# Performance work log

Measured on AMD Instinct MI355X. Metric: run time of the kernel, lower is better.

## Reference

```python
import jax, jax.numpy as jnp
import numpy as np

P = 65536          # collocation points
J = 16             # num_subdomains == pou num_partitions
WID = 64           # subnet width_size
N_SUB_HID = 2      # subnet depth=3 -> 2 extra hidden linear layers after the input layer
H = 64             # pou hidden_dim
N_POU_RES = 4      # pou depth=6 -> 4 residual blocks


def setup_inputs() -> dict:
    key = jax.random.key(0)
    ks = jax.random.split(key, 14)
    s = 0.1  # small init scale for stable tanh/softmax
    return {
        "x": jax.random.uniform(ks[0], (P, 2), jnp.float32),
        "sub_W0": s * jax.random.normal(ks[1], (J, 2, WID), jnp.float32),
        "sub_b0": s * jax.random.normal(ks[2], (J, WID), jnp.float32),
        "sub_Wh": s * jax.random.normal(ks[3], (J, N_SUB_HID, WID, WID), jnp.float32),
        "sub_bh": s * jax.random.normal(ks[4], (J, N_SUB_HID, WID), jnp.float32),
        "sub_Wl": s * jax.random.normal(ks[5], (J, WID, 1), jnp.float32),
        "sub_bl": s * jax.random.normal(ks[6], (J, 1), jnp.float32),
        "pou_W0": s * jax.random.normal(ks[7], (2, H), jnp.float32),
        "pou_b0": s * jax.random.normal(ks[8], (H,), jnp.float32),
        "pou_Wh": s * jax.random.normal(ks[9], (N_POU_RES, H, H), jnp.float32),
        "pou_bh": s * jax.random.normal(ks[10], (N_POU_RES, H), jnp.float32),
        "pou_Wl": s * jax.random.normal(ks[11], (H, J), jnp.float32),
        "pou_bl": s * jax.random.normal(ks[12], (J,), jnp.float32),
    }


def reference(x, sub_W0, sub_b0, sub_Wh, sub_bh, sub_Wl, sub_bl,
              pou_W0, pou_b0, pou_Wh, pou_bh, pou_Wl, pou_bl):
    x = jnp.atleast_2d(x)
    # --- ResPOUNet2D.forward: partition-of-unity weights (computed ONCE, not per j) ---
    h = jax.nn.relu(x @ pou_W0 + pou_b0)                      # [P, H]
    for i in range(pou_Wh.shape[0]):                          # residual relu blocks
        h = h + jax.nn.relu(h @ pou_Wh[i] + pou_bh[i])
    w_all = jax.nn.softmax(h @ pou_Wl + pou_bl, axis=-1)      # [P, J]
    # --- batched subnets: eqx.nn.MLP with tanh, applied to (x-0.5)*2 ---
    xs = (x - 0.5) * 2.0                                      # [P, 2]
    hs = jnp.tanh(jnp.einsum('pd,jdw->jpw', xs, sub_W0) + sub_b0[:, None, :])  # [J, P, W]
    for i in range(sub_Wh.shape[1]):
        hs = jnp.tanh(jnp.einsum('jpw,jwv->jpv', hs, sub_Wh[:, i]) + sub_bh[:, i][:, None, :])
    u = (jnp.einsum('jpw,jwo->jpo', hs, sub_Wl) + sub_bl[:, None, :])[..., 0]  # [J, P]
    # --- weighted sum over subdomains ---
    total = jnp.einsum('pj,jp->p', w_all, u)                  # [P]
    # --- ansatz: hard zero-Dirichlet BC on unit square ---
    return total * jnp.sin(jnp.pi * x[:, 0]) * jnp.sin(jnp.pi * x[:, 1])
```

## Files before the change

kernel.cpp:

```cpp
#include <hip/hip_runtime.h>
#include <math.h>

#define NP 65536
#define NJ 16
#define WID 64
#define HH 64
#define NPOU 4
#define NSUB 2
#define L2E2 2.8853900817779268f

typedef __attribute__((ext_vector_type(8))) short short8;
typedef __attribute__((ext_vector_type(4))) float f32x4;
typedef __attribute__((ext_vector_type(4))) int int4v;

#define CHUNK_US(row, chunk) ((((row) << 6)) + ((((chunk) ^ ((row) & 7))) << 3))
__device__ __forceinline__ int usIdx(int row, int col) {
    return ((row) << 6) + ((((col >> 3) ^ (row & 7))) << 3) + (col & 7);
}

__device__ __forceinline__ unsigned short f2bf(float f) {
    unsigned u = __float_as_uint(f);
    u += 0x7FFFu + ((u >> 16) & 1u);
    return (unsigned short)(u >> 16);
}
__device__ __forceinline__ unsigned short rhu(float f) {
    return (unsigned short)((__float_as_uint(f) + 0x8000u) >> 16);
}
__device__ __forceinline__ unsigned pk2(float a, float b) {
    unsigned ua = __float_as_uint(a) + 0x8000u;
    unsigned ub = __float_as_uint(b) + 0x8000u;
    return __builtin_amdgcn_perm(ub, ua, 0x07060302u);
}
__device__ __forceinline__ unsigned cvtpk(float a, float b) {
    unsigned r;
    asm("v_cvt_pk_bf16_f32 %0, %1, %2" : "=v"(r) : "v"(a), "v"(b));
    return r;
}
__device__ __forceinline__ float bf2f(unsigned short s) {
    return __uint_as_float(((unsigned)s) << 16);
}
__device__ __forceinline__ float tanh2(float y) {
    float e = __builtin_amdgcn_exp2f(y);
    return fmaf(-2.0f, __builtin_amdgcn_rcpf(e + 1.0f), 1.0f);
}
__device__ __forceinline__ short8 mk8(unsigned a, unsigned b, unsigned c, unsigned d) {
    int4v t; t.x = (int)a; t.y = (int)b; t.z = (int)c; t.w = (int)d;
    return __builtin_bit_cast(short8, t);
}
#define CB_TRANSFORM(hsrc, bfdst)                                              \
    {                                                                          \
        _Pragma("unroll")                                                      \
        for (int kn = 0; kn < 2; ++kn) {                                       \
            unsigned A0 = cvtpk(hsrc[2 * kn][0],     hsrc[2 * kn][1]);         \
            unsigned A1 = cvtpk(hsrc[2 * kn][2],     hsrc[2 * kn][3]);         \
            unsigned B0 = cvtpk(hsrc[2 * kn + 1][0], hsrc[2 * kn + 1][1]);     \
            unsigned B1 = cvtpk(hsrc[2 * kn + 1][2], hsrc[2 * kn + 1][3]);     \
            asm("v_permlane32_swap_b32 %0, %1" : "+v"(A0), "+v"(B0));          \
            asm("v_permlane16_swap_b32 %0, %1" : "+v"(A0), "+v"(B0));          \
            asm("v_permlane32_swap_b32 %0, %1" : "+v"(A1), "+v"(B1));          \
            asm("v_permlane16_swap_b32 %0, %1" : "+v"(A1), "+v"(B1));          \
            bfdst[kn] = mk8(A0, A1, B0, B1);                                   \
        }                                                                      \
    }

__global__ __launch_bounds__(256) void prep_all_kernel(
    const float* __restrict__ sW0, const float* __restrict__ sb0,
    const float* __restrict__ sWh, const float* __restrict__ sbh_,
    const float* __restrict__ sWl, const float* __restrict__ sbl,
    const float* __restrict__ pW0, const float* __restrict__ pb0,
    const float* __restrict__ pWh, const float* __restrict__ pbh,
    const float* __restrict__ pWl, const float* __restrict__ pbl,
    int4v* __restrict__ wfrag, float* __restrict__ prm,
    int4v* __restrict__ pwf,   float* __restrict__ pp)
{
    const int blk = blockIdx.x;
    const int tid = threadIdx.x;

    if (blk < 64) {
        const int j  = blk >> 2;
        const int bx = blk & 3;
        const int f  = bx * 256 + tid;
        const int lane = f & 63, kc = (f >> 6) & 1, mt = (f >> 7) & 3, L = f >> 9;
        const int c = lane & 15, g = lane >> 4;
        const int n = mt * 16 + c;

        const float* src = sWh + j * (NSUB * WID * WID) + L * 4096;
        unsigned w[4];
#pragma unroll
        for (int e2 = 0; e2 < 4; ++e2) {
            int k = kc * 32 + 8 * g + 2 * e2;
            float v0 = L2E2 * src[k * 64 + n];
            float v1 = L2E2 * src[(k + 1) * 64 + n];
            w[e2] = (unsigned)f2bf(v0) | ((unsigned)f2bf(v1) << 16);
        }
        int4v r; r.x = (int)w[0]; r.y = (int)w[1]; r.z = (int)w[2]; r.w = (int)w[3];
        wfrag[j * 1024 + f] = r;

        if (bx == 0) {
            float* pj = prm + j * 512;
            if (tid < WID) {
                float w0 = sW0[j * 2 * WID + tid], w1 = sW0[j * 2 * WID + WID + tid];
                pj[tid]       = 2.0f * L2E2 * w0;
                pj[64 + tid]  = 2.0f * L2E2 * w1;
                pj[128 + tid] = L2E2 * (sb0[j * WID + tid] - w0 - w1);
            }
            if (tid < NSUB * WID) pj[192 + tid] = L2E2 * sbh_[j * NSUB * WID + tid];
            if (tid < WID) pj[320 + tid] = sWl[j * WID + tid];
            if (tid == 0) pj[384] = sbl[j];
        }
    } else {
        const int pb = blk - 64;
        const int idx = pb * 256 + tid;

        if (idx < 2048) {
            const int r = idx >> 9, mt = (idx >> 7) & 3, kc = (idx >> 6) & 1, lane = idx & 63;
            const int c = lane & 15, g = lane >> 4;
            const int n = mt * 16 + c;
            const float* src = pWh + r * 4096;
            unsigned w[4];
#pragma unroll
            for (int e2 = 0; e2 < 4; ++e2) {
                int k = kc * 32 + 8 * g + 2 * e2;
                w[e2] = (unsigned)f2bf(src[k * 64 + n]) | ((unsigned)f2bf(src[(k + 1) * 64 + n]) << 16);
            }
            int4v rr; rr.x = (int)w[0]; rr.y = (int)w[1]; rr.z = (int)w[2]; rr.w = (int)w[3];
            pwf[idx] = rr;
        } else if (idx < 2176) {
            const int t = idx - 2048;
            const int kc = t >> 6, lane = t & 63;
            const int jj = lane & 15, g = lane >> 4;
            unsigned w[4];
#pragma unroll
            for (int e2 = 0; e2 < 4; ++e2) {
                int k = kc * 32 + 8 * g + 2 * e2;
                w[e2] = (unsigned)f2bf(pWl[k * 16 + jj]) | ((unsigned)f2bf(pWl[(k + 1) * 16 + jj]) << 16);
            }
            int4v rr; rr.x = (int)w[0]; rr.y = (int)w[1]; rr.z = (int)w[2]; rr.w = (int)w[3];
            pwf[idx] = rr;
        }
        if (pb == 8) {
            if (tid < HH) {
                pp[tid]       = pW0[tid];
                pp[64 + tid]  = pW0[HH + tid];
                pp[128 + tid] = pb0[tid];
            }
            pp[192 + tid] = pbh[tid];
            if (tid < NJ) pp[448 + tid] = pbl[tid];
        }
    }
}

__global__ __launch_bounds__(256) void pou16_kernel(
    const float* __restrict__ x,
    const short8* __restrict__ pwf, const float* __restrict__ pp,
    float* __restrict__ w_all)
{
    const int tid = threadIdx.x, wave = tid >> 6, lane = tid & 63;
    const int c = lane & 15, g = lane >> 4;
    const int pb = blockIdx.x * 64 + wave * 16;

    float2 xv = ((const float2*)x)[pb + c];

    float trunk[4][4];
#pragma unroll
    for (int mt = 0; mt < 4; ++mt) {
        f32x4 a  = *(const f32x4*)&pp[      mt * 16 + 4 * g];
        f32x4 b  = *(const f32x4*)&pp[ 64 + mt * 16 + 4 * g];
        f32x4 bb = *(const f32x4*)&pp[128 + mt * 16 + 4 * g];
#pragma unroll
        for (int q = 0; q < 4; ++q)
            trunk[mt][q] = fmaxf(fmaf(xv.x, a[q], fmaf(xv.y, b[q], bb[q])), 0.0f);
    }

#pragma unroll
    for (int r = 0; r < NPOU; ++r) {
        short8 bf[2];
        CB_TRANSFORM(trunk, bf);
        f32x4 acc[4];
#pragma unroll
        for (int mt = 0; mt < 4; ++mt)
            acc[mt] = *(const f32x4*)&pp[192 + r * 64 + mt * 16 + 4 * g];
#pragma unroll
        for (int mt = 0; mt < 4; ++mt) {
            short8 a0 = pwf[((r * 4 + mt) * 2 + 0) * 64 + lane];
            short8 a1 = pwf[((r * 4 + mt) * 2 + 1) * 64 + lane];
            acc[mt] = __builtin_amdgcn_mfma_f32_16x16x32_bf16(a0, bf[0], acc[mt], 0, 0, 0);
            acc[mt] = __builtin_amdgcn_mfma_f32_16x16x32_bf16(a1, bf[1], acc[mt], 0, 0, 0);
        }
#pragma unroll
        for (int mt = 0; mt < 4; ++mt)
#pragma unroll
            for (int q = 0; q < 4; ++q)
                trunk[mt][q] += fmaxf(acc[mt][q], 0.0f);
    }

    short8 bfl[2];
    CB_TRANSFORM(trunk, bfl);
    f32x4 lac = *(const f32x4*)&pp[448 + 4 * g];
    lac = __builtin_amdgcn_mfma_f32_16x16x32_bf16(pwf[2048 + lane],      bfl[0], lac, 0, 0, 0);
    lac = __builtin_amdgcn_mfma_f32_16x16x32_bf16(pwf[2048 + 64 + lane], bfl[1], lac, 0, 0, 0);

    float m = fmaxf(fmaxf(lac[0], lac[1]), fmaxf(lac[2], lac[3]));
    m = fmaxf(m, __shfl_xor(m, 16));
    m = fmaxf(m, __shfl_xor(m, 32));
    float ev[4]; float s = 0.0f;
#pragma unroll
    for (int q = 0; q < 4; ++q) { ev[q] = __expf(lac[q] - m); s += ev[q]; }
    s += __shfl_xor(s, 16);
    s += __shfl_xor(s, 32);
    const float ss = __builtin_amdgcn_sinf(xv.x * 0.5f) * __builtin_amdgcn_sinf(xv.y * 0.5f);
    const float f = __builtin_amdgcn_rcpf(s) * ss;
#pragma unroll
    for (int q = 0; q < 4; ++q)
        w_all[(4 * g + q) * NP + pb + c] = ev[q] * f;
}

__global__ __launch_bounds__(256, 4) void subnet_nolds_kernel(
    const float* __restrict__ x,
    const short8* __restrict__ wfrag,
    const float* __restrict__ prm,
    const float* __restrict__ w_all,
    float* __restrict__ out)
{
    const int tid  = threadIdx.x;
    const int j    = blockIdx.y;
    const int wave = tid >> 6;
    const int lane = tid & 63;
    const int c    = lane & 15;
    const int g    = lane >> 4;

    const float*  pj = prm + j * 512;
    const short8* wf = wfrag + j * 1024;
    const int pb = blockIdx.x * 256 + wave * 64;

    short8 bf[2][4];
    {
        float xs0[4], xs1[4];
#pragma unroll
        for (int nt = 0; nt < 4; ++nt) {
            float2 xv = ((const float2*)x)[pb + nt * 16 + c];
            xs0[nt] = xv.x; xs1[nt] = xv.y;
        }
        f32x4 wa[2][2], wb[2][2], bb[2][2];
#pragma unroll
        for (int kc = 0; kc < 2; ++kc)
#pragma unroll
            for (int hf = 0; hf < 2; ++hf) {
                wa[kc][hf] = *(const f32x4*)&pj[      kc * 32 + 8 * g + 4 * hf];
                wb[kc][hf] = *(const f32x4*)&pj[ 64 + kc * 32 + 8 * g + 4 * hf];
                bb[kc][hf] = *(const f32x4*)&pj[128 + kc * 32 + 8 * g + 4 * hf];
            }
        unsigned t[2][4][4];
#pragma unroll
        for (int kc = 0; kc < 2; ++kc)
#pragma unroll
            for (int pr = 0; pr < 4; ++pr) {
                const int h0 = pr >> 1, e0 = (2 * pr) & 3, e1 = e0 + 1;
#pragma unroll
                for (int nt = 0; nt < 4; ++nt) {
                    float v0 = tanh2(fmaf(xs0[nt], wa[kc][h0][e0], fmaf(xs1[nt], wb[kc][h0][e0], bb[kc][h0][e0])));
                    float v1 = tanh2(fmaf(xs0[nt], wa[kc][h0][e1], fmaf(xs1[nt], wb[kc][h0][e1], bb[kc][h0][e1])));
                    t[kc][nt][pr] = cvtpk(v0, v1);
                }
            }
#pragma unroll
        for (int kc = 0; kc < 2; ++kc)
#pragma unroll
            for (int nt = 0; nt < 4; ++nt)
                bf[kc][nt] = mk8(t[kc][nt][0], t[kc][nt][1], t[kc][nt][2], t[kc][nt][3]);
    }

    float red[4];
#pragma unroll
    for (int nt = 0; nt < 4; ++nt) red[nt] = 0.0f;

#pragma unroll
    for (int L = 0; L < NSUB; ++L) {
        short8 aw[4][2];
#pragma unroll
        for (int mt = 0; mt < 4; ++mt)
#pragma unroll
            for (int kc = 0; kc < 2; ++kc)
                aw[mt][kc] = wf[((L * 4 + mt) * 2 + kc) * 64 + lane];
        f32x4 bias[4];
#pragma unroll
        for (int mt = 0; mt < 4; ++mt)
            bias[mt] = *(const f32x4*)&pj[192 + L * 64 + mt * 16 + 4 * g];

#pragma unroll
        for (int nt = 0; nt < 4; ++nt) {
            f32x4 acc[4];
#pragma unroll
            for (int mt = 0; mt < 4; ++mt) acc[mt] = bias[mt];
#pragma unroll
            for (int mt = 0; mt < 4; ++mt) {
                acc[mt] = __builtin_amdgcn_mfma_f32_16x16x32_bf16(aw[mt][0], bf[0][nt], acc[mt], 0, 0, 0);
                acc[mt] = __builtin_amdgcn_mfma_f32_16x16x32_bf16(aw[mt][1], bf[1][nt], acc[mt], 0, 0, 0);
            }

            if (L < NSUB - 1) {
                float h[4][4];
#pragma unroll
                for (int mt = 0; mt < 4; ++mt)
#pragma unroll
                    for (int q = 0; q < 4; ++q) h[mt][q] = tanh2(acc[mt][q]);
                short8 btmp[2];
                CB_TRANSFORM(h, btmp);
                bf[0][nt] = btmp[0];
                bf[1][nt] = btmp[1];
            } else {
#pragma unroll
                for (int mt = 0; mt < 4; ++mt) {
                    f32x4 wlv = *(const f32x4*)&pj[320 + mt * 16 + 4 * g];
#pragma unroll
                    for (int q = 0; q < 4; ++q)
                        red[nt] = fmaf(tanh2(acc[mt][q]), wlv[q], red[nt]);
                }
            }
        }
    }

#pragma unroll
    for (int nt = 0; nt < 4; ++nt) {
        red[nt] += __shfl_xor(red[nt], 16);
        red[nt] += __shfl_xor(red[nt], 32);
    }
    float u = (g & 1) ? ((g & 2) ? red[3] : red[1]) : ((g & 2) ? red[2] : red[0]);
    u += pj[384];

    const int p = pb + lane;
    atomicAdd(&out[p], u * w_all[j * NP + p]);
}

__global__ __launch_bounds__(256) void pou_mfma_kernel(
    const float* __restrict__ x,
    const float* __restrict__ W0, const float* __restrict__ b0,
    const float* __restrict__ Wh, const float* __restrict__ bh,
    const float* __restrict__ Wl, const float* __restrict__ bl,
    float* __restrict__ w_all)
{
    __shared__ unsigned short sA[4 * 64 * 64];
    __shared__ unsigned short sWhT[NPOU * 64 * 64];
    __shared__ unsigned short sWlT[16 * 64];
    __shared__ float sW0a[HH], sW0b[HH], sB0[HH];
    __shared__ float sbh[NPOU * HH];
    __shared__ float sbl[NJ];

    const int tid  = threadIdx.x;
    const int wave = tid >> 6;
    const int lane = tid & 63;
    const int r15  = lane & 15;
    const int g    = lane >> 4;

    for (int idx = tid; idx < NPOU * HH * HH; idx += 256) {
        int r = idx >> 12, k = (idx >> 6) & 63, n = idx & 63;
        sWhT[r * 4096 + usIdx(n, k)] = f2bf(Wh[idx]);
    }
    for (int idx = tid; idx < HH * NJ; idx += 256) {
        int k = idx >> 4, j = idx & 15;
        sWlT[usIdx(j, k)] = f2bf(Wl[idx]);
    }
    if (tid < HH) { sW0a[tid] = W0[tid]; sW0b[tid] = W0[HH + tid]; sB0[tid] = b0[tid]; }
    for (int i = tid; i < NPOU * HH; i += 256) sbh[i] = bh[i];
    if (tid < NJ) sbl[tid] = bl[tid];
    __syncthreads();

    unsigned short* myA = &sA[wave * 4096];
    const int pbase = blockIdx.x * 256;

    {
        const int p = pbase + tid;
        float2 xv = ((const float2*)x)[p];
        float v[HH];
#pragma unroll
        for (int c = 0; c < HH; ++c)
            v[c] = fmaxf(fmaf(xv.x, sW0a[c], fmaf(xv.y, sW0b[c], sB0[c])), 0.0f);
#pragma unroll
        for (int c = 0; c < 8; ++c) {
            int4v r;
            r.x = (int)pk2(v[8 * c + 0], v[8 * c + 1]);
            r.y = (int)pk2(v[8 * c + 2], v[8 * c + 3]);
            r.z = (int)pk2(v[8 * c + 4], v[8 * c + 5]);
            r.w = (int)pk2(v[8 * c + 6], v[8 * c + 7]);
            *(int4v*)&myA[CHUNK_US(lane, c)] = r;
        }
    }

    float trunk[4][4][4];
#pragma unroll
    for (int mt = 0; mt < 4; ++mt)
#pragma unroll
        for (int nt = 0; nt < 4; ++nt)
#pragma unroll
            for (int q = 0; q < 4; ++q)
                trunk[mt][nt][q] = bf2f(myA[usIdx(mt * 16 + g * 4 + q, nt * 16 + r15)]);

#pragma unroll 1
    for (int r = 0; r < NPOU; ++r) {
        const unsigned short* wt = &sWhT[r * 4096];
        short8 bfr[2][4];
#pragma unroll
        for (int kc = 0; kc < 2; ++kc)
#pragma unroll
            for (int nt = 0; nt < 4; ++nt)
                bfr[kc][nt] = *(const short8*)&wt[CHUNK_US(nt * 16 + r15, kc * 4 + g)];
        float bias[4];
#pragma unroll
        for (int nt = 0; nt < 4; ++nt) bias[nt] = sbh[r * HH + nt * 16 + r15];

#pragma unroll
        for (int mt = 0; mt < 4; ++mt) {
            short8 a0 = *(const short8*)&myA[CHUNK_US(mt * 16 + r15, g)];
            short8 a1 = *(const short8*)&myA[CHUNK_US(mt * 16 + r15, 4 + g)];
            f32x4 acc[4];
#pragma unroll
            for (int nt = 0; nt < 4; ++nt) {
                acc[nt] = (f32x4)(0.0f);
                acc[nt] = __builtin_amdgcn_mfma_f32_16x16x32_bf16(a0, bfr[0][nt], acc[nt], 0, 0, 0);
                acc[nt] = __builtin_amdgcn_mfma_f32_16x16x32_bf16(a1, bfr[1][nt], acc[nt], 0, 0, 0);
            }
#pragma unroll
            for (int nt = 0; nt < 4; ++nt)
#pragma unroll
                for (int q = 0; q < 4; ++q) {
                    float t = trunk[mt][nt][q] + fmaxf(acc[nt][q] + bias[nt], 0.0f);
                    trunk[mt][nt][q] = t;
                    myA[usIdx(mt * 16 + g * 4 + q, nt * 16 + r15)] = rhu(t);
                }
        }
    }

    short8 bw0 = *(const short8*)&sWlT[CHUNK_US(r15, g)];
    short8 bw1 = *(const short8*)&sWlT[CHUNK_US(r15, 4 + g)];
    float lg[4][4], mx[4][4];
#pragma unroll
    for (int mt = 0; mt < 4; ++mt) {
        short8 a0 = *(const short8*)&myA[CHUNK_US(mt * 16 + r15, g)];
        short8 a1 = *(const short8*)&myA[CHUNK_US(mt * 16 + r15, 4 + g)];
        f32x4 acc = (f32x4)(0.0f);
        acc = __builtin_amdgcn_mfma_f32_16x16x32_bf16(a0, bw0, acc, 0, 0, 0);
        acc = __builtin_amdgcn_mfma_f32_16x16x32_bf16(a1, bw1, acc, 0, 0, 0);
#pragma unroll
        for (int q = 0; q < 4; ++q) { lg[mt][q] = acc[q] + sbl[r15]; mx[mt][q] = lg[mt][q]; }
    }
#pragma unroll
    for (int mask = 1; mask < 16; mask <<= 1)
#pragma unroll
        for (int mt = 0; mt < 4; ++mt)
#pragma unroll
            for (int q = 0; q < 4; ++q) mx[mt][q] = fmaxf(mx[mt][q], __shfl_xor(mx[mt][q], mask));
    float ev[4][4], sm[4][4];
#pragma unroll
    for (int mt = 0; mt < 4; ++mt)
#pragma unroll
        for (int q = 0; q < 4; ++q) { ev[mt][q] = __expf(lg[mt][q] - mx[mt][q]); sm[mt][q] = ev[mt][q]; }
#pragma unroll
    for (int mask = 1; mask < 16; mask <<= 1)
#pragma unroll
        for (int mt = 0; mt < 4; ++mt)
#pragma unroll
            for (int q = 0; q < 4; ++q) sm[mt][q] += __shfl_xor(sm[mt][q], mask);
#pragma unroll
    for (int mt = 0; mt < 4; ++mt)
#pragma unroll
        for (int q = 0; q < 4; ++q) {
            const int p = pbase + wave * 64 + mt * 16 + g * 4 + q;
            w_all[r15 * NP + p] = ev[mt][q] * __builtin_amdgcn_rcpf(sm[mt][q]);
        }
}

__global__ __launch_bounds__(256) void subnet_mfma_fallback(
    const float* __restrict__ x,
    const float* __restrict__ gW0, const float* __restrict__ gb0,
    const float* __restrict__ gWh, const float* __restrict__ gbh,
    const float* __restrict__ gWl, const float* __restrict__ gbl,
    const float* __restrict__ w_all,
    float* __restrict__ upart)
{
    __shared__ __align__(16) unsigned short sWt[NSUB * 64 * 64];
    __shared__ __align__(16) float sW0a[WID], sW0b[WID], sB0[WID];
    __shared__ __align__(16) float sbh[NSUB * WID];
    __shared__ __align__(16) float sWl[WID];
    __shared__ float sbl1v;

    const int tid  = threadIdx.x;
    const int j    = blockIdx.y;
    const int wave = tid >> 6;
    const int lane = tid & 63;
    const int c    = lane & 15;
    const int g    = lane >> 4;

    {
        const float* src = gWh + j * (NSUB * WID * WID);
        for (int idx = tid; idx < NSUB * WID * WID; idx += 256) {
            int L = idx >> 12, rem = idx & 4095;
            int k = rem >> 6, n = rem & 63;
            sWt[L * 4096 + usIdx(n, k)] = f2bf(L2E2 * src[idx]);
        }
        if (tid < WID) {
            float w0 = gW0[j * 2 * WID + tid], w1 = gW0[j * 2 * WID + WID + tid];
            sW0a[tid] = 2.0f * L2E2 * w0;
            sW0b[tid] = 2.0f * L2E2 * w1;
            sB0[tid]  = L2E2 * (gb0[j * WID + tid] - w0 - w1);
        }
        if (tid < NSUB * WID) sbh[tid] = L2E2 * gbh[j * NSUB * WID + tid];
        if (tid < WID) sWl[tid] = gWl[j * WID + tid];
        if (tid == 0) sbl1v = gbl[j];
    }
    __syncthreads();

    const int pb = blockIdx.x * 256 + wave * 64;

    short8 bf[2][4];
    {
        float xs0[4], xs1[4];
#pragma unroll
        for (int nt = 0; nt < 4; ++nt) {
            float2 xv = ((const float2*)x)[pb + nt * 16 + c];
            xs0[nt] = xv.x; xs1[nt] = xv.y;
        }
        f32x4 wa[2][2], wb[2][2], bb[2][2];
#pragma unroll
        for (int kc = 0; kc < 2; ++kc)
#pragma unroll
            for (int hf = 0; hf < 2; ++hf) {
                wa[kc][hf] = *(const f32x4*)&sW0a[kc * 32 + 8 * g + 4 * hf];
                wb[kc][hf] = *(const f32x4*)&sW0b[kc * 32 + 8 * g + 4 * hf];
                bb[kc][hf] = *(const f32x4*)&sB0 [kc * 32 + 8 * g + 4 * hf];
            }
        unsigned t[2][4][4];
#pragma unroll
        for (int kc = 0; kc < 2; ++kc)
#pragma unroll
            for (int pr = 0; pr < 4; ++pr) {
                const int h0 = pr >> 1, e0 = (2 * pr) & 3, e1 = e0 + 1;
#pragma unroll
                for (int nt = 0; nt < 4; ++nt) {
                    float v0 = tanh2(fmaf(xs0[nt], wa[kc][h0][e0], fmaf(xs1[nt], wb[kc][h0][e0], bb[kc][h0][e0])));
                    float v1 = tanh2(fmaf(xs0[nt], wa[kc][h0][e1], fmaf(xs1[nt], wb[kc][h0][e1], bb[kc][h0][e1])));
                    t[kc][nt][pr] = cvtpk(v0, v1);
                }
            }
#pragma unroll
        for (int kc = 0; kc < 2; ++kc)
#pragma unroll
            for (int nt = 0; nt < 4; ++nt)
                bf[kc][nt] = mk8(t[kc][nt][0], t[kc][nt][1], t[kc][nt][2], t[kc][nt][3]);
    }

    float red[4];
#pragma unroll
    for (int nt = 0; nt < 4; ++nt) red[nt] = 0.0f;

#pragma unroll
    for (int L = 0; L < NSUB; ++L) {
        const unsigned short* wt = &sWt[L * 4096];
        short8 aw[4][2];
#pragma unroll
        for (int mt = 0; mt < 4; ++mt)
#pragma unroll
            for (int kc = 0; kc < 2; ++kc)
                aw[mt][kc] = *(const short8*)&wt[CHUNK_US(mt * 16 + c, kc * 4 + g)];
        f32x4 bias[4];
#pragma unroll
        for (int mt = 0; mt < 4; ++mt)
            bias[mt] = *(const f32x4*)&sbh[L * 64 + mt * 16 + 4 * g];

#pragma unroll
        for (int nt = 0; nt < 4; ++nt) {
            f32x4 acc[4];
#pragma unroll
            for (int mt = 0; mt < 4; ++mt) acc[mt] = bias[mt];
#pragma unroll
            for (int mt = 0; mt < 4; ++mt) {
                acc[mt] = __builtin_amdgcn_mfma_f32_16x16x32_bf16(aw[mt][0], bf[0][nt], acc[mt], 0, 0, 0);
                acc[mt] = __builtin_amdgcn_mfma_f32_16x16x32_bf16(aw[mt][1], bf[1][nt], acc[mt], 0, 0, 0);
            }

            if (L < NSUB - 1) {
                float h[4][4];
#pragma unroll
                for (int mt = 0; mt < 4; ++mt)
#pragma unroll
                    for (int q = 0; q < 4; ++q) h[mt][q] = tanh2(acc[mt][q]);
                short8 btmp[2];
                CB_TRANSFORM(h, btmp);
                bf[0][nt] = btmp[0];
                bf[1][nt] = btmp[1];
            } else {
#pragma unroll
                for (int mt = 0; mt < 4; ++mt) {
                    f32x4 wlv = *(const f32x4*)&sWl[mt * 16 + 4 * g];
#pragma unroll
                    for (int q = 0; q < 4; ++q)
                        red[nt] = fmaf(tanh2(acc[mt][q]), wlv[q], red[nt]);
                }
            }
        }
    }

#pragma unroll
    for (int nt = 0; nt < 4; ++nt) {
        red[nt] += __shfl_xor(red[nt], 16);
        red[nt] += __shfl_xor(red[nt], 32);
    }
    float u = (g & 1) ? ((g & 2) ? red[3] : red[1]) : ((g & 2) ? red[2] : red[0]);
    u += sbl1v;

    const int p = pb + lane;
    upart[j * NP + p] = u * w_all[j * NP + p];
}

__global__ __launch_bounds__(256) void reduce_kernel(
    const float* __restrict__ x,
    const float* __restrict__ upart,
    float* __restrict__ out)
{
    const int p = blockIdx.x * 256 + threadIdx.x;
    float s = 0.0f;
#pragma unroll
    for (int j = 0; j < NJ; ++j) s += upart[j * NP + p];
    float2 xv = ((const float2*)x)[p];
    float s0 = __builtin_amdgcn_sinf(xv.x * 0.5f);
    float s1 = __builtin_amdgcn_sinf(xv.y * 0.5f);
    out[p] = s * s0 * s1;
}

extern "C" void kernel_launch(void* const* d_in, const int* in_sizes, int n_in,
                              void* d_out, int out_size, void* d_ws, size_t ws_size,
                              hipStream_t stream) {
    const float* x      = (const float*)d_in[0];
    const float* sub_W0 = (const float*)d_in[1];
    const float* sub_b0 = (const float*)d_in[2];
    const float* sub_Wh = (const float*)d_in[3];
    const float* sub_bh = (const float*)d_in[4];
    const float* sub_Wl = (const float*)d_in[5];
    const float* sub_bl = (const float*)d_in[6];
    const float* pou_W0 = (const float*)d_in[7];
    const float* pou_b0 = (const float*)d_in[8];
    const float* pou_Wh = (const float*)d_in[9];
    const float* pou_bh = (const float*)d_in[10];
    const float* pou_Wl = (const float*)d_in[11];
    const float* pou_bl = (const float*)d_in[12];

    float* w_all = (float*)d_ws;
    float* upart = (float*)d_ws + (size_t)NJ * NP;
    char*  extra  = (char*)d_ws + (size_t)2 * NJ * NP * 4;
    void*  swf    = (void*)extra;
    float* sprm   = (float*)(extra + (size_t)NJ * 1024 * 16);
    char*  extra2 = extra + (size_t)NJ * 1024 * 16 + (size_t)NJ * 512 * 4;
    void*  pwf    = (void*)extra2;
    float* pprm   = (float*)(extra2 + 2176 * 16);

    const size_t need = (size_t)2 * NJ * NP * 4 + (size_t)NJ * 1024 * 16
                      + (size_t)NJ * 512 * 4 + 2176 * 16 + 512 * 4;
    const bool use_prep = (ws_size >= need);

    if (use_prep) {
        hipMemsetAsync(d_out, 0, (size_t)out_size * sizeof(float), stream);
        prep_all_kernel<<<73, 256, 0, stream>>>(sub_W0, sub_b0, sub_Wh, sub_bh, sub_Wl, sub_bl,
                                                pou_W0, pou_b0, pou_Wh, pou_bh, pou_Wl, pou_bl,
                                                (int4v*)swf, sprm, (int4v*)pwf, pprm);
        pou16_kernel<<<NP / 64, 256, 0, stream>>>(x, (const short8*)pwf, pprm, w_all);
        dim3 g2(NP / 256, NJ);
        subnet_nolds_kernel<<<g2, 256, 0, stream>>>(x, (const short8*)swf, sprm, w_all,
                                                    (float*)d_out);
    } else {
        pou_mfma_kernel<<<NP / 256, 256, 0, stream>>>(x, pou_W0, pou_b0, pou_Wh, pou_bh,
                                                      pou_Wl, pou_bl, w_all);
        dim3 g2(NP / 256, NJ);
        subnet_mfma_fallback<<<g2, 256, 0, stream>>>(x, sub_W0, sub_b0, sub_Wh, sub_bh,
                                                     sub_Wl, sub_bl, w_all, upart);
        reduce_kernel<<<NP / 256, 256, 0, stream>>>(x, upart, (float*)d_out);
    }
}
```

Measured before the change: 70.13 us.

## Compute subnet input layer with MFMA using split-bf16 weights, fold memset into pou kernel

The subnet's first layer (2-input linear plus tanh) moves from scalar FMAs to a 16x16x32 bf16 MFMA. Both x and the input weights are split into hi/lo bf16 parts to keep roughly fp32 accuracy, and a new prep section builds the packed weight fragments. The output zeroing moves from a separate hipMemsetAsync into the pou kernel, which removes one launch. The trade is extra MFMA issue and permlane transforms in place of VALU work, plus small precision differences from the split-bf16 trick.

```diff
diff --git a/kernel.cpp b/kernel.cpp
--- a/kernel.cpp
+++ b/kernel.cpp
@@ -71,7 +71,8 @@
     const float* __restrict__ pWh, const float* __restrict__ pbh,
     const float* __restrict__ pWl, const float* __restrict__ pbl,
     int4v* __restrict__ wfrag, float* __restrict__ prm,
-    int4v* __restrict__ pwf,   float* __restrict__ pp)
+    int4v* __restrict__ pwf,   float* __restrict__ pp,
+    int4v* __restrict__ wfrag0)
 {
     const int blk = blockIdx.x;
     const int tid = threadIdx.x;
@@ -108,7 +109,7 @@
             if (tid < WID) pj[320 + tid] = sWl[j * WID + tid];
             if (tid == 0) pj[384] = sbl[j];
         }
-    } else {
+    } else if (blk < 73) {
         const int pb = blk - 64;
         const int idx = pb * 256 + tid;
 
@@ -147,17 +148,38 @@
             pp[192 + tid] = pbh[tid];
             if (tid < NJ) pp[448 + tid] = pbl[tid];
         }
+    } else {
+        const int t = (blk - 73) * 256 + tid;
+        const int j = t >> 8, rem = t & 255;
+        const int mt = rem >> 6, lane = rem & 63;
+        const int c = lane & 15, g = lane >> 4;
+        const int n = mt * 16 + c;
+        unsigned r0 = 0, r1 = 0, r2 = 0;
+        if (g == 0) {
+            float w0c = 2.0f * L2E2 * sW0[j * 2 * WID + n];
+            float w1c = 2.0f * L2E2 * sW0[j * 2 * WID + WID + n];
+            unsigned short h0 = f2bf(w0c), h1 = f2bf(w1c);
+            unsigned short l0 = f2bf(w0c - bf2f(h0));
+            unsigned short l1 = f2bf(w1c - bf2f(h1));
+            r0 = (unsigned)h0 | ((unsigned)h1 << 16);
+            r1 = r0;
+            r2 = (unsigned)l0 | ((unsigned)l1 << 16);
+        }
+        int4v rr; rr.x = (int)r0; rr.y = (int)r1; rr.z = (int)r2; rr.w = 0;
+        wfrag0[j * 256 + mt * 64 + lane] = rr;
     }
 }
 
 __global__ __launch_bounds__(256) void pou16_kernel(
     const float* __restrict__ x,
     const short8* __restrict__ pwf, const float* __restrict__ pp,
-    float* __restrict__ w_all)
+    float* __restrict__ w_all, float* __restrict__ outz)
 {
     const int tid = threadIdx.x, wave = tid >> 6, lane = tid & 63;
     const int c = lane & 15, g = lane >> 4;
     const int pb = blockIdx.x * 64 + wave * 16;
+
+    if (tid < 16) ((f32x4*)outz)[blockIdx.x * 16 + tid] = (f32x4)(0.0f);
 
     float2 xv = ((const float2*)x)[pb + c];
 
@@ -218,6 +240,7 @@
 __global__ __launch_bounds__(256, 4) void subnet_nolds_kernel(
     const float* __restrict__ x,
     const short8* __restrict__ wfrag,
+    const short8* __restrict__ wfrag0,
     const float* __restrict__ prm,
     const float* __restrict__ w_all,
     float* __restrict__ out)
@@ -229,45 +252,43 @@
     const int c    = lane & 15;
     const int g    = lane >> 4;
 
-    const float*  pj = prm + j * 512;
-    const short8* wf = wfrag + j * 1024;
+    const float*  pj  = prm + j * 512;
+    const short8* wf  = wfrag + j * 1024;
+    const short8* wf0 = wfrag0 + j * 256;
     const int pb = blockIdx.x * 256 + wave * 64;
 
+    short8 aw0[4];
+#pragma unroll
+    for (int mt = 0; mt < 4; ++mt) aw0[mt] = wf0[mt * 64 + lane];
+    f32x4 bias0[4];
+#pragma unroll
+    for (int mt = 0; mt < 4; ++mt)
+        bias0[mt] = *(const f32x4*)&pj[128 + mt * 16 + 4 * g];
+
     short8 bf[2][4];
-    {
-        float xs0[4], xs1[4];
-#pragma unroll
-        for (int nt = 0; nt < 4; ++nt) {
-            float2 xv = ((const float2*)x)[pb + nt * 16 + c];
-            xs0[nt] = xv.x; xs1[nt] = xv.y;
-        }
-        f32x4 wa[2][2], wb[2][2], bb[2][2];
-#pragma unroll
-        for (int kc = 0; kc < 2; ++kc)
-#pragma unroll
-            for (int hf = 0; hf < 2; ++hf) {
-                wa[kc][hf] = *(const f32x4*)&pj[      kc * 32 + 8 * g + 4 * hf];
-                wb[kc][hf] = *(const f32x4*)&pj[ 64 + kc * 32 + 8 * g + 4 * hf];
-                bb[kc][hf] = *(const f32x4*)&pj[128 + kc * 32 + 8 * g + 4 * hf];
-            }
-        unsigned t[2][4][4];
-#pragma unroll
-        for (int kc = 0; kc < 2; ++kc)
-#pragma unroll
-            for (int pr = 0; pr < 4; ++pr) {
-                const int h0 = pr >> 1, e0 = (2 * pr) & 3, e1 = e0 + 1;
-#pragma unroll
-                for (int nt = 0; nt < 4; ++nt) {
-                    float v0 = tanh2(fmaf(xs0[nt], wa[kc][h0][e0], fmaf(xs1[nt], wb[kc][h0][e0], bb[kc][h0][e0])));
-                    float v1 = tanh2(fmaf(xs0[nt], wa[kc][h0][e1], fmaf(xs1[nt], wb[kc][h0][e1], bb[kc][h0][e1])));
-                    t[kc][nt][pr] = cvtpk(v0, v1);
-                }
-            }
-#pragma unroll
-        for (int kc = 0; kc < 2; ++kc)
-#pragma unroll
-            for (int nt = 0; nt < 4; ++nt)
-                bf[kc][nt] = mk8(t[kc][nt][0], t[kc][nt][1], t[kc][nt][2], t[kc][nt][3]);
+#pragma unroll
+    for (int nt = 0; nt < 4; ++nt) {
+        float2 xv = ((const float2*)x)[pb + nt * 16 + c];
+        unsigned r0 = cvtpk(xv.x, xv.y);
+        float x0l = xv.x - __uint_as_float(r0 << 16);
+        float x1l = xv.y - __uint_as_float(r0 & 0xffff0000u);
+        unsigned r1 = cvtpk(x0l, x1l);
+        short8 bx = mk8(r0, r1, r0, 0u);
+
+        f32x4 acc[4];
+#pragma unroll
+        for (int mt = 0; mt < 4; ++mt)
+            acc[mt] = __builtin_amdgcn_mfma_f32_16x16x32_bf16(aw0[mt], bx, bias0[mt], 0, 0, 0);
+
+        float h[4][4];
+#pragma unroll
+        for (int mt = 0; mt < 4; ++mt)
+#pragma unroll
+            for (int q = 0; q < 4; ++q) h[mt][q] = tanh2(acc[mt][q]);
+        short8 btmp[2];
+        CB_TRANSFORM(h, btmp);
+        bf[0][nt] = btmp[0];
+        bf[1][nt] = btmp[1];
     }
 
     float red[4];
@@ -651,20 +672,23 @@
     char*  extra2 = extra + (size_t)NJ * 1024 * 16 + (size_t)NJ * 512 * 4;
     void*  pwf    = (void*)extra2;
     float* pprm   = (float*)(extra2 + 2176 * 16);
+    void*  swf0   = (void*)(extra2 + 2176 * 16 + 512 * 4);
 
     const size_t need = (size_t)2 * NJ * NP * 4 + (size_t)NJ * 1024 * 16
-                      + (size_t)NJ * 512 * 4 + 2176 * 16 + 512 * 4;
+                      + (size_t)NJ * 512 * 4 + 2176 * 16 + 512 * 4
+                      + (size_t)NJ * 256 * 16;
     const bool use_prep = (ws_size >= need);
 
     if (use_prep) {
-        hipMemsetAsync(d_out, 0, (size_t)out_size * sizeof(float), stream);
-        prep_all_kernel<<<73, 256, 0, stream>>>(sub_W0, sub_b0, sub_Wh, sub_bh, sub_Wl, sub_bl,
+        prep_all_kernel<<<89, 256, 0, stream>>>(sub_W0, sub_b0, sub_Wh, sub_bh, sub_Wl, sub_bl,
                                                 pou_W0, pou_b0, pou_Wh, pou_bh, pou_Wl, pou_bl,
-                                                (int4v*)swf, sprm, (int4v*)pwf, pprm);
-        pou16_kernel<<<NP / 64, 256, 0, stream>>>(x, (const short8*)pwf, pprm, w_all);
+                                                (int4v*)swf, sprm, (int4v*)pwf, pprm,
+                                                (int4v*)swf0);
+        pou16_kernel<<<NP / 64, 256, 0, stream>>>(x, (const short8*)pwf, pprm, w_all,
+                                                  (float*)d_out);
         dim3 g2(NP / 256, NJ);
-        subnet_nolds_kernel<<<g2, 256, 0, stream>>>(x, (const short8*)swf, sprm, w_all,
-                                                    (float*)d_out);
+        subnet_nolds_kernel<<<g2, 256, 0, stream>>>(x, (const short8*)swf, (const short8*)swf0,
+                                                    sprm, w_all, (float*)d_out);
     } else {
         pou_mfma_kernel<<<NP / 256, 256, 0, stream>>>(x, pou_W0, pou_b0, pou_Wh, pou_bh,
                                                       pou_Wl, pou_bl, w_all);
```

After: 68.05 us. 1.03x faster.
